# Optimization experiments

Measured on AMD Instinct MI355X. Metric: run time of the kernel, lower is better.

The kernel has to match this reference:

```python
import jax, jax.numpy as jnp
import numpy as np

K = 1024      # size_codebook
D = 64        # dim_codebook
N = 131072    # number of input vectors
GAMMA = 0.99
ALPHA = 1e-09
BETA = 0.25


def setup_inputs() -> dict:
    key = jax.random.key(0)
    k1, k2, k3 = jax.random.split(key, 3)
    X = jax.random.normal(k1, (N, D), dtype=jnp.float32)
    E = jax.random.normal(k2, (K, D), dtype=jnp.float32)
    cluster_sizes = jnp.zeros((K,), dtype=jnp.float32)
    moving_avg = E  # buffer initialized to a clone of E.weight
    return {"X": X, "E": E, "cluster_sizes": cluster_sizes, "moving_avg": moving_avg}


def reference(X, E, cluster_sizes, moving_avg):
    # squared euclidean distances: [N, K]
    X_sqnorm = jnp.sum(X * X, axis=1, keepdims=True)          # [N, 1]
    E_sqnorm = jnp.sum(E * E, axis=1)[None, :]                # [1, K]
    dist = X_sqnorm + E_sqnorm - 2.0 * (X @ E.T)              # [N, K]
    min_dist = jnp.min(dist, axis=1)                          # [N]
    argmins = jnp.argmin(dist, axis=1)                        # [N]
    Z_embs_raw = E[argmins]                                   # [N, D]

    # commitment loss (codebook is detached in the EMA variant)
    diff = X - jax.lax.stop_gradient(Z_embs_raw)
    loss = BETA * jnp.mean(jnp.sum(diff * diff, axis=1))

    # EMA codebook update (training mode, no-grad in torch)
    counts = jax.ops.segment_sum(jnp.ones((N,), dtype=X.dtype), argmins, num_segments=K)
    cs = GAMMA * cluster_sizes + (1.0 - GAMMA) * counts
    cs = (cs + ALPHA) / (1.0 + ALPHA * K / jnp.sum(cs))
    sums = jax.ops.segment_sum(X, argmins, num_segments=K)    # one_hot.T @ X, [K, D]
    ma = GAMMA * moving_avg + (1.0 - GAMMA) * sums
    E_new = ma / cs[:, None]

    # straight-through estimator
    Z_embs = X + jax.lax.stop_gradient(Z_embs_raw - X)
    return (Z_embs, loss, argmins, min_dist, E_new, cs, ma)
```

## Files before the change

### kernel.cpp

```cpp
#include <hip/hip_runtime.h>
#include <math.h>

#define NN 131072
#define KK 1024
#define DD 64
#define GAMMA 0.99f
#define ALPHA 1e-9f
#define BETA 0.25f

typedef float f32x4 __attribute__((ext_vector_type(4)));
typedef short bf16x8 __attribute__((ext_vector_type(8)));

__device__ __constant__ float OMG = (float)(1.0 - 0.99);

__device__ __forceinline__ void split_bf16(float v, unsigned short& h, unsigned short& l) {
    unsigned int b = __float_as_uint(v);
    unsigned int hb = b & 0xFFFF0000u;
    h = (unsigned short)(hb >> 16);
    float r = v - __uint_as_float(hb);
    unsigned int lb = __float_as_uint(r);
    lb += 0x7FFFu + ((lb >> 16) & 1u);
    l = (unsigned short)(lb >> 16);
}

__global__ __launch_bounds__(64)
void vq_prep(const float* __restrict__ E, float4* __restrict__ Efrag,
             float* __restrict__ esqh) {
    int nt = blockIdx.x;
    int l = threadIdx.x;
    int n = nt * 16 + (l & 15);
    int kb = (l >> 4) * 8;
    float ss = 0.f;
    #pragma unroll
    for (int ks = 0; ks < 2; ++ks) {
        const float4* xp = (const float4*)(E + (size_t)n * DD + ks * 32 + kb);
        float4 a = xp[0], b = xp[1];
        float v[8] = {a.x, a.y, a.z, a.w, b.x, b.y, b.z, b.w};
        union { float4 f; unsigned short u[8]; } H, L;
        #pragma unroll
        for (int j = 0; j < 8; ++j) {
            unsigned short hh, ll;
            split_bf16(v[j], hh, ll);
            H.u[j] = hh; L.u[j] = ll;
            ss = fmaf(v[j], v[j], ss);
        }
        int fid = nt * 4 + ks * 2;
        Efrag[(size_t)(fid + 0) * 64 + l] = H.f;
        Efrag[(size_t)(fid + 1) * 64 + l] = L.f;
    }
    ss += __shfl_xor(ss, 16, 64);
    ss += __shfl_xor(ss, 32, 64);
    if (l < 16) esqh[nt * 16 + l] = -0.5f * ss;
}

#define BM 64

__global__ __launch_bounds__(256, 4)
void vq_main(const float* __restrict__ X, const float* __restrict__ E,
             const float4* __restrict__ Efrag, const float* __restrict__ esqh,
             float* __restrict__ argf, float* __restrict__ mind,
             float* __restrict__ Z, int* __restrict__ cursor,
             int* __restrict__ rowlist, float* __restrict__ sumsFB,
             float* __restrict__ loss_part, int cap) {
    __shared__ float redv[128];
    __shared__ int redi[128];
    __shared__ int bidx[64];
    __shared__ float bsc[64];
    __shared__ float xsqs[64];
    __shared__ int fbflag[64];

    int tid = threadIdx.x;
    int lane = tid & 63, w = tid >> 6;
    int rg = w & 1, cg = w >> 1;
    int lc = lane & 15, lq = lane >> 4;

    size_t bb = (size_t)blockIdx.x * BM;
    size_t R0 = bb + rg * 32;

    bf16x8 ah[2][2], al[2][2];
    #pragma unroll
    for (int mt = 0; mt < 2; ++mt) {
        float xq = 0.f;
        #pragma unroll
        for (int ks = 0; ks < 2; ++ks) {
            const float4* xp =
                (const float4*)(X + (R0 + mt * 16 + lc) * DD + ks * 32 + lq * 8);
            float4 x0 = xp[0], x1 = xp[1];
            float v[8] = {x0.x, x0.y, x0.z, x0.w, x1.x, x1.y, x1.z, x1.w};
            union { bf16x8 s; unsigned short u[8]; } H, L;
            #pragma unroll
            for (int j = 0; j < 8; ++j) {
                unsigned short hh, ll;
                split_bf16(v[j], hh, ll);
                H.u[j] = hh; L.u[j] = ll;
                xq = fmaf(v[j], v[j], xq);
            }
            ah[mt][ks] = H.s;
            al[mt][ks] = L.s;
        }
        xq += __shfl_xor(xq, 16, 64);
        xq += __shfl_xor(xq, 32, 64);
        if (lane < 16) xsqs[rg * 32 + mt * 16 + lane] = xq;
    }

    float bestv[2][4];
    int besti[2][4];
    #pragma unroll
    for (int mt = 0; mt < 2; ++mt)
        #pragma unroll
        for (int r = 0; r < 4; ++r) { bestv[mt][r] = -3.402823466e38f; besti[mt][r] = 0; }

    const float4* bp = Efrag + (size_t)(cg * 32) * 256 + lane;
    const float* ep = esqh + cg * 512 + lc;

    int st = (blockIdx.x >> 3) & 31;

    int p0 = st;
    int p1 = (st + 1) & 31;
    const float4* q0 = bp + (size_t)p0 * 256;
    const float4* q1 = bp + (size_t)p1 * 256;
    float4 na0 = q0[0], na1 = q0[64], na2 = q0[128], na3 = q0[192];
    float ea = ep[p0 * 16];
    float4 mb0 = q1[0], mb1 = q1[64], mb2 = q1[128], mb3 = q1[192];
    float eb = ep[p1 * 16];

    for (int i = 0; i < 32; i += 2) {
        {
            int ntp = (i + st) & 31;
            union { float4 f; bf16x8 s; } u0, u1, u2, u3;
            u0.f = na0; u1.f = na1; u2.f = na2; u3.f = na3;
            float ec = ea;
            if (i + 2 < 32) {
                int np = (i + 2 + st) & 31;
                const float4* q = bp + (size_t)np * 256;
                na0 = q[0]; na1 = q[64]; na2 = q[128]; na3 = q[192];
                ea = ep[np * 16];
            }
            f32x4 acc[2];
            #pragma unroll
            for (int mt = 0; mt < 2; ++mt) acc[mt] = (f32x4){ec, ec, ec, ec};
            #pragma unroll
            for (int mt = 0; mt < 2; ++mt)
                acc[mt] = __builtin_amdgcn_mfma_f32_16x16x32_bf16(ah[mt][0], u0.s, acc[mt], 0, 0, 0);
            #pragma unroll
            for (int mt = 0; mt < 2; ++mt)
                acc[mt] = __builtin_amdgcn_mfma_f32_16x16x32_bf16(ah[mt][1], u2.s, acc[mt], 0, 0, 0);
            #pragma unroll
            for (int mt = 0; mt < 2; ++mt)
                acc[mt] = __builtin_amdgcn_mfma_f32_16x16x32_bf16(ah[mt][0], u1.s, acc[mt], 0, 0, 0);
            #pragma unroll
            for (int mt = 0; mt < 2; ++mt)
                acc[mt] = __builtin_amdgcn_mfma_f32_16x16x32_bf16(ah[mt][1], u3.s, acc[mt], 0, 0, 0);
            #pragma unroll
            for (int mt = 0; mt < 2; ++mt)
                acc[mt] = __builtin_amdgcn_mfma_f32_16x16x32_bf16(al[mt][0], u0.s, acc[mt], 0, 0, 0);
            #pragma unroll
            for (int mt = 0; mt < 2; ++mt)
                acc[mt] = __builtin_amdgcn_mfma_f32_16x16x32_bf16(al[mt][1], u2.s, acc[mt], 0, 0, 0);
            int n = cg * 512 + ntp * 16 + lc;
            #pragma unroll
            for (int mt = 0; mt < 2; ++mt)
                #pragma unroll
                for (int r = 0; r < 4; ++r) {
                    float sc = acc[mt][r];
                    if (sc > bestv[mt][r]) { bestv[mt][r] = sc; besti[mt][r] = n; }
                }
        }
        {
            int ntp = (i + 1 + st) & 31;
            union { float4 f; bf16x8 s; } u0, u1, u2, u3;
            u0.f = mb0; u1.f = mb1; u2.f = mb2; u3.f = mb3;
            float ec = eb;
            if (i + 3 < 32) {
                int np = (i + 3 + st) & 31;
                const float4* q = bp + (size_t)np * 256;
                mb0 = q[0]; mb1 = q[64]; mb2 = q[128]; mb3 = q[192];
                eb = ep[np * 16];
            }
            f32x4 acc[2];
            #pragma unroll
            for (int mt = 0; mt < 2; ++mt) acc[mt] = (f32x4){ec, ec, ec, ec};
            #pragma unroll
            for (int mt = 0; mt < 2; ++mt)
                acc[mt] = __builtin_amdgcn_mfma_f32_16x16x32_bf16(ah[mt][0], u0.s, acc[mt], 0, 0, 0);
            #pragma unroll
            for (int mt = 0; mt < 2; ++mt)
                acc[mt] = __builtin_amdgcn_mfma_f32_16x16x32_bf16(ah[mt][1], u2.s, acc[mt], 0, 0, 0);
            #pragma unroll
            for (int mt = 0; mt < 2; ++mt)
                acc[mt] = __builtin_amdgcn_mfma_f32_16x16x32_bf16(ah[mt][0], u1.s, acc[mt], 0, 0, 0);
            #pragma unroll
            for (int mt = 0; mt < 2; ++mt)
                acc[mt] = __builtin_amdgcn_mfma_f32_16x16x32_bf16(ah[mt][1], u3.s, acc[mt], 0, 0, 0);
            #pragma unroll
            for (int mt = 0; mt < 2; ++mt)
                acc[mt] = __builtin_amdgcn_mfma_f32_16x16x32_bf16(al[mt][0], u0.s, acc[mt], 0, 0, 0);
            #pragma unroll
            for (int mt = 0; mt < 2; ++mt)
                acc[mt] = __builtin_amdgcn_mfma_f32_16x16x32_bf16(al[mt][1], u2.s, acc[mt], 0, 0, 0);
            int n = cg * 512 + ntp * 16 + lc;
            #pragma unroll
            for (int mt = 0; mt < 2; ++mt)
                #pragma unroll
                for (int r = 0; r < 4; ++r) {
                    float sc = acc[mt][r];
                    if (sc > bestv[mt][r]) { bestv[mt][r] = sc; besti[mt][r] = n; }
                }
        }
    }

    #pragma unroll
    for (int off = 1; off <= 8; off <<= 1) {
        #pragma unroll
        for (int mt = 0; mt < 2; ++mt) {
            #pragma unroll
            for (int r = 0; r < 4; ++r) {
                float ov = __shfl_xor(bestv[mt][r], off, 64);
                int oi = __shfl_xor(besti[mt][r], off, 64);
                if (ov > bestv[mt][r] || (ov == bestv[mt][r] && oi < besti[mt][r])) {
                    bestv[mt][r] = ov; besti[mt][r] = oi;
                }
            }
        }
    }
    if (lc == 0) {
        #pragma unroll
        for (int mt = 0; mt < 2; ++mt)
            #pragma unroll
            for (int r = 0; r < 4; ++r) {
                int row = rg * 32 + mt * 16 + lq * 4 + r;
                redv[row * 2 + cg] = bestv[mt][r];
                redi[row * 2 + cg] = besti[mt][r];
            }
    }
    __syncthreads();
    if (tid < 64) {
        float v0 = redv[tid * 2], v1 = redv[tid * 2 + 1];
        int i0 = redi[tid * 2], i1 = redi[tid * 2 + 1];
        int pick = (v1 > v0 || (v1 == v0 && i1 < i0));
        bidx[tid] = pick ? i1 : i0;
        bsc[tid] = pick ? v1 : v0;
    }
    __syncthreads();

    if (tid < 64) {
        int row = tid;
        int bi = bidx[row];
        size_t grow = bb + row;
        float md = fmaf(-2.f, bsc[row], xsqs[row]);
        mind[grow] = md;
        argf[grow] = (float)bi;
        int pos = atomicAdd(&cursor[bi], 1);
        if (pos < cap) {
            rowlist[(size_t)bi * cap + pos] = (int)grow;
            fbflag[row] = 0;
        } else {
            fbflag[row] = 1;
        }
        #pragma unroll
        for (int m = 32; m; m >>= 1) md += __shfl_xor(md, m, 64);
        if (tid == 0) atomicAdd(&loss_part[blockIdx.x & 1023], md);
    }
    __syncthreads();

    #pragma unroll 4
    for (int it = 0; it < 16; ++it) {
        int row = w * 16 + it;
        int bi = bidx[row];
        size_t grow = bb + row;
        float e = E[(size_t)bi * DD + lane];
        Z[grow * DD + lane] = e;
        if (fbflag[row]) {
            float x = X[grow * DD + lane];
            atomicAdd(&sumsFB[(size_t)bi * DD + lane], x);
        }
    }
}

__global__ __launch_bounds__(1024)
void vq_sum_ema(const float* __restrict__ X, const int* __restrict__ rowlist,
                const int* __restrict__ cursor, const float* __restrict__ sumsFB,
                const float* __restrict__ cluster_sizes,
                const float* __restrict__ loss_part, const float* __restrict__ mavg,
                float* __restrict__ o_ma, float* __restrict__ o_enew,
                float* __restrict__ o_cs, float* __restrict__ o_loss, int cap) {
    __shared__ float part[16][64];
    __shared__ float redt[16];
    int k = blockIdx.x;
    int lane = threadIdx.x & 63, w = threadIdx.x >> 6;

    float t = GAMMA * cluster_sizes[threadIdx.x] + OMG * (float)cursor[threadIdx.x];
    #pragma unroll
    for (int m = 32; m; m >>= 1) t += __shfl_xor(t, m, 64);
    if (lane == 0) redt[w] = t;
    __syncthreads();
    float total = 0.f;
    #pragma unroll
    for (int j = 0; j < 16; ++j) total += redt[j];

    float csr = GAMMA * cluster_sizes[k] + OMG * (float)cursor[k];
    float cs = (csr + ALPHA) / (1.0f + (ALPHA * (float)KK) / total);
    if (threadIdx.x == 0) o_cs[k] = cs;

    if (k == 0) {
        __syncthreads();
        float t2 = loss_part[threadIdx.x];
        #pragma unroll
        for (int m = 32; m; m >>= 1) t2 += __shfl_xor(t2, m, 64);
        if (lane == 0) redt[w] = t2;
        __syncthreads();
        if (threadIdx.x == 0) {
            float l = 0.f;
            #pragma unroll
            for (int j = 0; j < 16; ++j) l += redt[j];
            o_loss[0] = BETA * (l / (float)NN);
        }
    }

    int cnt = cursor[k];
    int nr = cnt < cap ? cnt : cap;
    const int* rl = rowlist + (size_t)k * cap;
    float acc = 0.f;
    #pragma unroll 4
    for (int i = w; i < nr; i += 16) {
        int r = rl[i];
        acc += X[(size_t)r * DD + lane];
    }
    part[w][lane] = acc;
    __syncthreads();
    if (w == 0) {
        float s = sumsFB[(size_t)k * DD + lane];
        #pragma unroll
        for (int j = 0; j < 16; ++j) s += part[j][lane];
        float ma = GAMMA * mavg[(size_t)k * DD + lane] + OMG * s;
        o_ma[(size_t)k * DD + lane] = ma;
        o_enew[(size_t)k * DD + lane] = ma / cs;
    }
}

extern "C" void kernel_launch(void* const* d_in, const int* in_sizes, int n_in,
                              void* d_out, int out_size, void* d_ws, size_t ws_size,
                              hipStream_t stream) {
    const float* X = (const float*)d_in[0];
    const float* E = (const float*)d_in[1];
    const float* cluster_sizes = (const float*)d_in[2];
    const float* moving_avg = (const float*)d_in[3];

    float* out = (float*)d_out;
    float* o_Z = out;
    float* o_loss = o_Z + (size_t)NN * DD;
    float* o_arg = o_loss + 1;
    float* o_mind = o_arg + NN;
    float* o_enew = o_mind + NN;
    float* o_cs = o_enew + (size_t)KK * DD;
    float* o_ma = o_cs + KK;

    int* cursor = (int*)d_ws;
    float* loss_part = (float*)d_ws + 1024;
    float* sumsFB = loss_part + 1024;
    float* esqh = sumsFB + (size_t)KK * DD;
    float4* Efrag = (float4*)(esqh + KK);
    int* rowlist = (int*)(esqh + KK + (size_t)KK * DD);

    size_t base_bytes = (size_t)(1024 + 1024 + KK * DD + KK + KK * DD) * 4;
    long cap_l = ((long)ws_size - (long)base_bytes) / (long)(KK * sizeof(int));
    int cap = cap_l < 0 ? 0 : (cap_l > 1024 ? 1024 : (int)cap_l);

    hipMemsetAsync(d_ws, 0, (size_t)(1024 + 1024 + KK * DD) * 4, stream);

    vq_prep<<<KK / 16, 64, 0, stream>>>(E, Efrag, esqh);
    vq_main<<<NN / BM, 256, 0, stream>>>(X, E, Efrag, esqh, o_arg, o_mind, o_Z,
                                         cursor, rowlist, sumsFB, loss_part, cap);
    vq_sum_ema<<<KK, 1024, 0, stream>>>(X, rowlist, cursor, sumsFB, cluster_sizes,
                                        loss_part, moving_avg, o_ma, o_enew,
                                        o_cs, o_loss, cap);
}
```

Measured before the change: 203.1 us.

## Stage codebook fragments into LDS via async global_load_lds double buffering

Replaces the per-wave register prefetch of codebook fragments with a block-wide double-buffered LDS staging scheme that uses global_load_lds. Each of the four waves loads a quarter of a tile, which is then shared by the two row-group waves of the same column group, halving global/L2 traffic for the codebook. The cost is two __syncthreads per tile pair and LDS reads in the inner loop. There is also no explicit wait on vmcnt for the async loads before consumption, so correctness relies on the barrier ordering.

```diff
diff --git a/kernel.cpp b/kernel.cpp
--- a/kernel.cpp
+++ b/kernel.cpp
@@ -10,6 +10,9 @@
 
 typedef float f32x4 __attribute__((ext_vector_type(4)));
 typedef short bf16x8 __attribute__((ext_vector_type(8)));
+
+typedef const __attribute__((address_space(1))) void gv_t;
+typedef __attribute__((address_space(3))) void lv_t;
 
 __device__ __constant__ float OMG = (float)(1.0 - 0.99);
 
@@ -62,6 +65,7 @@
              float* __restrict__ Z, int* __restrict__ cursor,
              int* __restrict__ rowlist, float* __restrict__ sumsFB,
              float* __restrict__ loss_part, int cap) {
+    __shared__ float4 stg[2][8][64];
     __shared__ float redv[128];
     __shared__ int redi[128];
     __shared__ int bidx[64];
@@ -76,6 +80,19 @@
 
     size_t bb = (size_t)blockIdx.x * BM;
     size_t R0 = bb + rg * 32;
+
+    int st = (blockIdx.x >> 3) & 31;
+
+    auto stage_tile = [&](float4 (*sb)[64], int nt) {
+        int cgs = w >> 1, fp = (w & 1) * 2;
+        const float4* gp = Efrag + ((size_t)(cgs * 32 + nt)) * 256 + fp * 64 + lane;
+        __builtin_amdgcn_global_load_lds((gv_t*)gp,
+                                         (lv_t*)&sb[cgs * 4 + fp][0], 16, 0, 0);
+        __builtin_amdgcn_global_load_lds((gv_t*)(gp + 64),
+                                         (lv_t*)&sb[cgs * 4 + fp + 1][0], 16, 0, 0);
+    };
+
+    stage_tile(stg[0], st);
 
     bf16x8 ah[2][2], al[2][2];
     #pragma unroll
@@ -110,103 +127,53 @@
         #pragma unroll
         for (int r = 0; r < 4; ++r) { bestv[mt][r] = -3.402823466e38f; besti[mt][r] = 0; }
 
-    const float4* bp = Efrag + (size_t)(cg * 32) * 256 + lane;
     const float* ep = esqh + cg * 512 + lc;
 
-    int st = (blockIdx.x >> 3) & 31;
-
-    int p0 = st;
-    int p1 = (st + 1) & 31;
-    const float4* q0 = bp + (size_t)p0 * 256;
-    const float4* q1 = bp + (size_t)p1 * 256;
-    float4 na0 = q0[0], na1 = q0[64], na2 = q0[128], na3 = q0[192];
-    float ea = ep[p0 * 16];
-    float4 mb0 = q1[0], mb1 = q1[64], mb2 = q1[128], mb3 = q1[192];
-    float eb = ep[p1 * 16];
+    auto consume = [&](float4 (*sb)[64], int ntp) {
+        float ec = ep[ntp * 16];
+        union { float4 f; bf16x8 s; } u0, u1, u2, u3;
+        u0.f = sb[cg * 4 + 0][lane];
+        u1.f = sb[cg * 4 + 1][lane];
+        u2.f = sb[cg * 4 + 2][lane];
+        u3.f = sb[cg * 4 + 3][lane];
+        f32x4 acc[2];
+        #pragma unroll
+        for (int mt = 0; mt < 2; ++mt) acc[mt] = (f32x4){ec, ec, ec, ec};
+        #pragma unroll
+        for (int mt = 0; mt < 2; ++mt)
+            acc[mt] = __builtin_amdgcn_mfma_f32_16x16x32_bf16(ah[mt][0], u0.s, acc[mt], 0, 0, 0);
+        #pragma unroll
+        for (int mt = 0; mt < 2; ++mt)
+            acc[mt] = __builtin_amdgcn_mfma_f32_16x16x32_bf16(ah[mt][1], u2.s, acc[mt], 0, 0, 0);
+        #pragma unroll
+        for (int mt = 0; mt < 2; ++mt)
+            acc[mt] = __builtin_amdgcn_mfma_f32_16x16x32_bf16(ah[mt][0], u1.s, acc[mt], 0, 0, 0);
+        #pragma unroll
+        for (int mt = 0; mt < 2; ++mt)
+            acc[mt] = __builtin_amdgcn_mfma_f32_16x16x32_bf16(ah[mt][1], u3.s, acc[mt], 0, 0, 0);
+        #pragma unroll
+        for (int mt = 0; mt < 2; ++mt)
+            acc[mt] = __builtin_amdgcn_mfma_f32_16x16x32_bf16(al[mt][0], u0.s, acc[mt], 0, 0, 0);
+        #pragma unroll
+        for (int mt = 0; mt < 2; ++mt)
+            acc[mt] = __builtin_amdgcn_mfma_f32_16x16x32_bf16(al[mt][1], u2.s, acc[mt], 0, 0, 0);
+        int n = cg * 512 + ntp * 16 + lc;
+        #pragma unroll
+        for (int mt = 0; mt < 2; ++mt)
+            #pragma unroll
+            for (int r = 0; r < 4; ++r) {
+                float sc = acc[mt][r];
+                if (sc > bestv[mt][r]) { bestv[mt][r] = sc; besti[mt][r] = n; }
+            }
+    };
 
     for (int i = 0; i < 32; i += 2) {
-        {
-            int ntp = (i + st) & 31;
-            union { float4 f; bf16x8 s; } u0, u1, u2, u3;
-            u0.f = na0; u1.f = na1; u2.f = na2; u3.f = na3;
-            float ec = ea;
-            if (i + 2 < 32) {
-                int np = (i + 2 + st) & 31;
-                const float4* q = bp + (size_t)np * 256;
-                na0 = q[0]; na1 = q[64]; na2 = q[128]; na3 = q[192];
-                ea = ep[np * 16];
-            }
-            f32x4 acc[2];
-            #pragma unroll
-            for (int mt = 0; mt < 2; ++mt) acc[mt] = (f32x4){ec, ec, ec, ec};
-            #pragma unroll
-            for (int mt = 0; mt < 2; ++mt)
-                acc[mt] = __builtin_amdgcn_mfma_f32_16x16x32_bf16(ah[mt][0], u0.s, acc[mt], 0, 0, 0);
-            #pragma unroll
-            for (int mt = 0; mt < 2; ++mt)
-                acc[mt] = __builtin_amdgcn_mfma_f32_16x16x32_bf16(ah[mt][1], u2.s, acc[mt], 0, 0, 0);
-            #pragma unroll
-            for (int mt = 0; mt < 2; ++mt)
-                acc[mt] = __builtin_amdgcn_mfma_f32_16x16x32_bf16(ah[mt][0], u1.s, acc[mt], 0, 0, 0);
-            #pragma unroll
-            for (int mt = 0; mt < 2; ++mt)
-                acc[mt] = __builtin_amdgcn_mfma_f32_16x16x32_bf16(ah[mt][1], u3.s, acc[mt], 0, 0, 0);
-            #pragma unroll
-            for (int mt = 0; mt < 2; ++mt)
-                acc[mt] = __builtin_amdgcn_mfma_f32_16x16x32_bf16(al[mt][0], u0.s, acc[mt], 0, 0, 0);
-            #pragma unroll
-            for (int mt = 0; mt < 2; ++mt)
-                acc[mt] = __builtin_amdgcn_mfma_f32_16x16x32_bf16(al[mt][1], u2.s, acc[mt], 0, 0, 0);
-            int n = cg * 512 + ntp * 16 + lc;
-            #pragma unroll
-            for (int mt = 0; mt < 2; ++mt)
-                #pragma unroll
-                for (int r = 0; r < 4; ++r) {
-                    float sc = acc[mt][r];
-                    if (sc > bestv[mt][r]) { bestv[mt][r] = sc; besti[mt][r] = n; }
-                }
-        }
-        {
-            int ntp = (i + 1 + st) & 31;
-            union { float4 f; bf16x8 s; } u0, u1, u2, u3;
-            u0.f = mb0; u1.f = mb1; u2.f = mb2; u3.f = mb3;
-            float ec = eb;
-            if (i + 3 < 32) {
-                int np = (i + 3 + st) & 31;
-                const float4* q = bp + (size_t)np * 256;
-                mb0 = q[0]; mb1 = q[64]; mb2 = q[128]; mb3 = q[192];
-                eb = ep[np * 16];
-            }
-            f32x4 acc[2];
-            #pragma unroll
-            for (int mt = 0; mt < 2; ++mt) acc[mt] = (f32x4){ec, ec, ec, ec};
-            #pragma unroll
-            for (int mt = 0; mt < 2; ++mt)
-                acc[mt] = __builtin_amdgcn_mfma_f32_16x16x32_bf16(ah[mt][0], u0.s, acc[mt], 0, 0, 0);
-            #pragma unroll
-            for (int mt = 0; mt < 2; ++mt)
-                acc[mt] = __builtin_amdgcn_mfma_f32_16x16x32_bf16(ah[mt][1], u2.s, acc[mt], 0, 0, 0);
-            #pragma unroll
-            for (int mt = 0; mt < 2; ++mt)
-                acc[mt] = __builtin_amdgcn_mfma_f32_16x16x32_bf16(ah[mt][0], u1.s, acc[mt], 0, 0, 0);
-            #pragma unroll
-            for (int mt = 0; mt < 2; ++mt)
-                acc[mt] = __builtin_amdgcn_mfma_f32_16x16x32_bf16(ah[mt][1], u3.s, acc[mt], 0, 0, 0);
-            #pragma unroll
-            for (int mt = 0; mt < 2; ++mt)
-                acc[mt] = __builtin_amdgcn_mfma_f32_16x16x32_bf16(al[mt][0], u0.s, acc[mt], 0, 0, 0);
-            #pragma unroll
-            for (int mt = 0; mt < 2; ++mt)
-                acc[mt] = __builtin_amdgcn_mfma_f32_16x16x32_bf16(al[mt][1], u2.s, acc[mt], 0, 0, 0);
-            int n = cg * 512 + ntp * 16 + lc;
-            #pragma unroll
-            for (int mt = 0; mt < 2; ++mt)
-                #pragma unroll
-                for (int r = 0; r < 4; ++r) {
-                    float sc = acc[mt][r];
-                    if (sc > bestv[mt][r]) { bestv[mt][r] = sc; besti[mt][r] = n; }
-                }
-        }
+        __syncthreads();
+        stage_tile(stg[1], (i + 1 + st) & 31);
+        consume(stg[0], (i + st) & 31);
+        __syncthreads();
+        if (i + 2 < 32) stage_tile(stg[0], (i + 2 + st) & 31);
+        consume(stg[1], (i + 1 + st) & 31);
     }
 
     #pragma unroll
```

Result: no change. 202.8 us (-0.1%).
